# Kernel optimization log

Measured on AMD Instinct MI355X. Metric: run time of the kernel, lower is better.

The kernel has to match this reference:

```python
import jax, jax.numpy as jnp
import numpy as np
import math

B, S, D, H, FF, L, V = 4, 2048, 512, 8, 2048, 4, 256
WINDOW, STRIDE, NGLOBAL = 256, 128, 16  # sparse pattern: causal & (local | strided | global)


def setup_inputs() -> dict:
    key = jax.random.key(0)
    ks = jax.random.split(key, 12)
    g = lambda k, shp: jax.random.normal(k, shp, dtype=jnp.float32) * 0.02
    return {
        "src_tokens": jax.random.randint(ks[0], (B, S), 0, V, dtype=jnp.int32),
        "emb": g(ks[1], (V, D)),
        "b_out": jnp.zeros((V,), jnp.float32),
        "Wq": g(ks[2], (L, D, D)), "bq": jnp.zeros((L, D), jnp.float32),
        "Wk": g(ks[3], (L, D, D)), "bk": jnp.zeros((L, D), jnp.float32),
        "Wv": g(ks[4], (L, D, D)), "bv": jnp.zeros((L, D), jnp.float32),
        "Wo": g(ks[5], (L, D, D)), "bo": jnp.zeros((L, D), jnp.float32),
        "ln1_g": jnp.ones((L, D), jnp.float32), "ln1_b": jnp.zeros((L, D), jnp.float32),
        "W1": g(ks[6], (L, D, FF)), "b1": jnp.zeros((L, FF), jnp.float32),
        "W2": g(ks[7], (L, FF, D)), "b2": jnp.zeros((L, D), jnp.float32),
        "ln2_g": jnp.ones((L, D), jnp.float32), "ln2_b": jnp.zeros((L, D), jnp.float32),
    }


def _pos_enc(seq_len, d_model):
    pos = jnp.arange(seq_len, dtype=jnp.float32)[:, None]
    div = jnp.exp(jnp.arange(0, d_model, 2, dtype=jnp.float32) * (-math.log(10000.0) / d_model))
    pe = jnp.zeros((seq_len, d_model), jnp.float32)
    pe = pe.at[:, 0::2].set(jnp.sin(pos * div)).at[:, 1::2].set(jnp.cos(pos * div))
    return pe


def _ln(x, g, b):
    m = x.mean(-1, keepdims=True)
    v = ((x - m) ** 2).mean(-1, keepdims=True)
    return (x - m) * jax.lax.rsqrt(v + 1e-5) * g + b


def _sparse_mask(seq_len):
    i = jnp.arange(seq_len)[:, None]
    j = jnp.arange(seq_len)[None, :]
    causal = j <= i
    local = (i - j) < WINDOW
    strided = ((i - j) % STRIDE) == 0
    glob = j < NGLOBAL
    return causal & (local | strided | glob)  # [S, S] bool


def reference(src_tokens, emb, b_out, Wq, bq, Wk, bk, Wv, bv, Wo, bo,
              ln1_g, ln1_b, W1, b1, W2, b2, ln2_g, ln2_b):
    dh = D // H
    x = emb[src_tokens] * math.sqrt(D) + _pos_enc(S, D)  # [B,S,D] (dropout inactive at eval)
    mask = _sparse_mask(S)
    for l in range(L):
        q = (x @ Wq[l] + bq[l]).reshape(B, S, H, dh)
        k = (x @ Wk[l] + bk[l]).reshape(B, S, H, dh)
        v = (x @ Wv[l] + bv[l]).reshape(B, S, H, dh)
        scores = jnp.einsum('bihd,bjhd->bhij', q, k) / math.sqrt(dh)
        scores = jnp.where(mask, scores, jnp.float32(-1e9))
        attn = jax.nn.softmax(scores, axis=-1)
        o = jnp.einsum('bhij,bjhd->bihd', attn, v).reshape(B, S, D)
        x = _ln(x + o @ Wo[l] + bo[l], ln1_g[l], ln1_b[l])      # post-LN residual
        h = jax.nn.relu(x @ W1[l] + b1[l])
        x = _ln(x + h @ W2[l] + b2[l], ln2_g[l], ln2_b[l])
    return x @ emb.T + b_out  # tied output projection -> [B,S,V]
```

## Files before the change

kernel.cpp:

```cpp
#include <hip/hip_runtime.h>
#include <hip/hip_bf16.h>
#include <math.h>

#define B_  4
#define S_  2048
#define D_  512
#define H_  8
#define DH_ 64
#define FF_ 2048
#define L_  4
#define V_  256
#define NTOK (B_ * S_)
#define XN  ((size_t)NTOK * D_)

typedef __attribute__((ext_vector_type(8))) short bf16x8;
typedef __attribute__((ext_vector_type(4))) float f32x4;
typedef __attribute__((ext_vector_type(8))) unsigned short u16x8;
typedef __attribute__((ext_vector_type(4))) unsigned short u16x4;

typedef const __attribute__((address_space(1))) unsigned int* gptr_u32;
typedef __attribute__((address_space(3))) unsigned int* lptr_u32;

__device__ __forceinline__ float bf2f(unsigned short u) {
    return __uint_as_float((unsigned)u << 16);
}
__device__ __forceinline__ unsigned short f2bf_bits(float f) {
    __hip_bfloat16 t = __float2bfloat16(f);
    return *(unsigned short*)&t;
}

__global__ void pe_table_kernel(float* __restrict__ PE) {
    int s = blockIdx.x;
    int d = threadIdx.x * 2;
    float ang = (float)s * expf((float)d * (-logf(10000.0f) / (float)D_));
    PE[(size_t)s * D_ + d]     = sinf(ang);
    PE[(size_t)s * D_ + d + 1] = cosf(ang);
}

__global__ void embed_kernel(const int* __restrict__ tok,
                             const float* __restrict__ emb,
                             const float* __restrict__ PE,
                             float* __restrict__ X,
                             __hip_bfloat16* __restrict__ Xb) {
    int bs = blockIdx.x;
    int s = bs % S_;
    int t = tok[bs];
    const float scale = 22.62741699796952f;
    int d = threadIdx.x * 4;
    float4 e = *(const float4*)(emb + (size_t)t * D_ + d);
    float4 p = *(const float4*)(PE + (size_t)s * D_ + d);
    float4 v = make_float4(e.x * scale + p.x, e.y * scale + p.y,
                           e.z * scale + p.z, e.w * scale + p.w);
    *(float4*)(X + (size_t)bs * D_ + d) = v;
    u16x4 pk = { f2bf_bits(v.x), f2bf_bits(v.y), f2bf_bits(v.z), f2bf_bits(v.w) };
    *(u16x4*)((unsigned short*)Xb + (size_t)bs * D_ + d) = pk;
}

__global__ void transpose_conv_kernel(const float* __restrict__ W,
                                      __hip_bfloat16* __restrict__ Wt,
                                      int K, int N) {
    const float* Wl = W + (size_t)blockIdx.z * K * N;
    __hip_bfloat16* Wtl = Wt + (size_t)blockIdx.z * K * N;
    __shared__ float t[32][33];
    int k0 = blockIdx.y * 32, n0 = blockIdx.x * 32;
    int tx = threadIdx.x & 31, ty = threadIdx.x >> 5;
    #pragma unroll
    for (int q = 0; q < 4; ++q)
        t[ty + q * 8][tx] = Wl[(size_t)(k0 + ty + q * 8) * N + n0 + tx];
    __syncthreads();
    #pragma unroll
    for (int q = 0; q < 4; ++q)
        Wtl[(size_t)(n0 + ty + q * 8) * K + k0 + tx] =
            __float2bfloat16(t[tx][ty + q * 8]);
}

__global__ void transpose_qkv_kernel(const float* __restrict__ Wq,
                                     const float* __restrict__ Wk,
                                     const float* __restrict__ Wv,
                                     __hip_bfloat16* __restrict__ dst) {
    int z = blockIdx.z, l = z / 3, which = z % 3;
    const float* src = (which == 0 ? Wq : which == 1 ? Wk : Wv) + (size_t)l * D_ * D_;
    __hip_bfloat16* d = dst + (size_t)l * 1536 * D_ + (size_t)which * D_ * D_;
    __shared__ float t[32][33];
    int k0 = blockIdx.y * 32, n0 = blockIdx.x * 32;
    int tx = threadIdx.x & 31, ty = threadIdx.x >> 5;
    #pragma unroll
    for (int q = 0; q < 4; ++q)
        t[ty + q * 8][tx] = src[(size_t)(k0 + ty + q * 8) * D_ + n0 + tx];
    __syncthreads();
    #pragma unroll
    for (int q = 0; q < 4; ++q)
        d[(size_t)(n0 + ty + q * 8) * D_ + k0 + tx] =
            __float2bfloat16(t[tx][ty + q * 8]);
}

__global__ void conv_bf16_kernel(const float* __restrict__ in,
                                 __hip_bfloat16* __restrict__ out, int n) {
    int i = blockIdx.x * 256 + threadIdx.x;
    if (i < n) out[i] = __float2bfloat16(in[i]);
}

template <int BM, int RELU, int OUT_MODE>
__global__ __launch_bounds__(256)
void gemm_bf16_kernel(const __hip_bfloat16* __restrict__ A,
                      const __hip_bfloat16* __restrict__ Bt,
                      const float* __restrict__ bias0,
                      const float* __restrict__ bias1,
                      const float* __restrict__ bias2,
                      float* __restrict__ Cf,
                      __hip_bfloat16* __restrict__ Cb0,
                      __hip_bfloat16* __restrict__ Cb1,
                      __hip_bfloat16* __restrict__ Cb2,
                      __hip_bfloat16* __restrict__ CbT,
                      int M, int N, int K) {
    constexpr int MI = BM / 32;
    __shared__ unsigned short As[2][BM * 32];
    __shared__ unsigned short Bs[2][128 * 32];
    int tid = threadIdx.x;
    int lane = tid & 63, wid = tid >> 6;
    int wm = (wid >> 1) * (BM / 2), wn = (wid & 1) * 64;
    int g = lane >> 4, il = lane & 15;

    int gx = gridDim.x;
    int fid = blockIdx.x + gx * blockIdx.y;
    int cpx = (gx * gridDim.y) >> 3;
    int swz = (fid & 7) * cpx + (fid >> 3);
    int m0 = (swz / gx) * BM, n0 = (swz % gx) * 128;

    auto stage = [&](int buf, int k0) {
        #pragma unroll
        for (int q = 0; q < BM / 64; ++q) {
            int idx = q * 256 + tid;
            int r = idx >> 2, c = idx & 3;
            int csw = (c ^ r) & 3;
            const __hip_bfloat16* sa = A + (size_t)(m0 + r) * K + k0 + csw * 8;
            __builtin_amdgcn_global_load_lds((gptr_u32)(const void*)sa,
                                             (lptr_u32)(void*)&As[buf][idx * 8], 16, 0, 0);
        }
        #pragma unroll
        for (int q = 0; q < 2; ++q) {
            int idx = q * 256 + tid;
            int r = idx >> 2, c = idx & 3;
            int csw = (c ^ r) & 3;
            const __hip_bfloat16* sb = Bt + (size_t)(n0 + r) * K + k0 + csw * 8;
            __builtin_amdgcn_global_load_lds((gptr_u32)(const void*)sb,
                                             (lptr_u32)(void*)&Bs[buf][idx * 8], 16, 0, 0);
        }
    };

    f32x4 acc[MI][4] = {};
    int NT = K >> 5;
    stage(0, 0);

    for (int t = 0; t < NT; ++t) {
        int cur = t & 1;
        if (t + 1 < NT) {
            stage(cur ^ 1, (t + 1) << 5);
            if constexpr (BM == 128)
                asm volatile("s_waitcnt vmcnt(4)" ::: "memory");
            else
                asm volatile("s_waitcnt vmcnt(3)" ::: "memory");
        } else {
            asm volatile("s_waitcnt vmcnt(0)" ::: "memory");
        }
        __builtin_amdgcn_s_barrier();

        bf16x8 af[MI], bf[4];
        #pragma unroll
        for (int i = 0; i < MI; ++i) {
            int m = wm + i * 16 + il;
            af[i] = *(const bf16x8*)&As[cur][m * 32 + ((g ^ m) & 3) * 8];
        }
        #pragma unroll
        for (int j = 0; j < 4; ++j) {
            int n = wn + j * 16 + il;
            bf[j] = *(const bf16x8*)&Bs[cur][n * 32 + ((g ^ n) & 3) * 8];
        }
        #pragma unroll
        for (int i = 0; i < MI; ++i)
            #pragma unroll
            for (int j = 0; j < 4; ++j)
                acc[i][j] = __builtin_amdgcn_mfma_f32_16x16x32_bf16(
                    af[i], bf[j], acc[i][j], 0, 0, 0);

        __builtin_amdgcn_s_barrier();
    }

    if constexpr (OUT_MODE == 4) {
        int seg = n0 >> 9;
        const float* bias = seg == 0 ? bias0 : seg == 1 ? bias1 : bias2;
        __hip_bfloat16* Crow = seg == 0 ? Cb0 : seg == 1 ? Cb1 : Cb2;
        int nseg = n0 & 511;
        #pragma unroll
        for (int j = 0; j < 4; ++j) {
            int coll = nseg + wn + j * 16 + il;
            float bv = bias[coll];
            #pragma unroll
            for (int i = 0; i < MI; ++i) {
                int row0 = m0 + wm + i * 16 + g * 4;
                if (seg < 2) {
                    #pragma unroll
                    for (int r = 0; r < 4; ++r)
                        Crow[(size_t)(row0 + r) * 512 + coll] =
                            __float2bfloat16(acc[i][j][r] + bv);
                } else {
                    u16x4 pk;
                    #pragma unroll
                    for (int r = 0; r < 4; ++r) {
                        float v = acc[i][j][r] + bv;
                        Crow[(size_t)(row0 + r) * 512 + coll] = __float2bfloat16(v);
                        pk[r] = f2bf_bits(v);
                    }
                    int hh = coll >> 6, dh = coll & 63;
                    int bb = row0 >> 11, s0 = row0 & 2047;
                    *(u16x4*)(CbT + ((size_t)((bb * 8 + hh) * 64 + dh) * 2048 + s0)) = pk;
                }
            }
        }
    } else {
        #pragma unroll
        for (int j = 0; j < 4; ++j) {
            int col = n0 + wn + j * 16 + il;
            float bv = bias0[col];
            #pragma unroll
            for (int i = 0; i < MI; ++i) {
                #pragma unroll
                for (int r = 0; r < 4; ++r) {
                    int row = m0 + wm + i * 16 + g * 4 + r;
                    float v = acc[i][j][r] + bv;
                    if (RELU) v = fmaxf(v, 0.0f);
                    if (OUT_MODE == 1) Cb0[(size_t)row * N + col] = __float2bfloat16(v);
                    else               Cf[(size_t)row * N + col] = v;
                }
            }
        }
    }
}

__device__ __forceinline__ bf16x8 lds_frag(const unsigned short* base, int row, int chunk) {
    int byte = (row << 7) + (((chunk ^ (row & 7)) & 7) << 4);
    return *(const bf16x8*)((const char*)base + byte);
}

__global__ __launch_bounds__(256)
void attn_mfma_kernel(const __hip_bfloat16* __restrict__ Q,
                      const __hip_bfloat16* __restrict__ K,
                      const __hip_bfloat16* __restrict__ V,
                      const __hip_bfloat16* __restrict__ VT,
                      __hip_bfloat16* __restrict__ O) {
    __shared__ unsigned short SM[4096 + 4096 + 4096];
    unsigned short* Ks = SM;
    unsigned short* Vs = SM + 4096;

    int d = blockIdx.x + 32 * (blockIdx.y + 8 * blockIdx.z);
    int xcd = d & 7;
    int rest = d >> 3;
    int gsub = rest & 3;
    int qt = rest >> 2;
    int grp = xcd * 4 + gsub;
    int h = grp & 7, b = grp >> 3;
    int i0 = qt * 64;

    int tid = threadIdx.x, lane = tid & 63, wv = tid >> 6;
    int g = lane >> 4, il = lane & 15, g4 = g * 4;

    int nloc = min(i0 >> 6, 4) + 1;
    int add0 = (i0 > 256);
    int nt = nloc + add0;

    const size_t vt_off = (size_t)((b * 8 + h) * 64) * 2048;
    auto j0_of = [&](int t) { return (t < nloc) ? (i0 - 64 * t) : 0; };

    auto stage = [&](int j0) {
        #pragma unroll
        for (int q = 0; q < 2; ++q) {
            int idx = q * 256 + tid;
            int row = idx >> 3, c = idx & 7;
            int csw = c ^ (row & 7);
            const __hip_bfloat16* sk = K + (size_t)(b * 2048 + j0 + row) * 512 + h * 64 + csw * 8;
            __builtin_amdgcn_global_load_lds((gptr_u32)(const void*)sk,
                                             (lptr_u32)(void*)&Ks[idx * 8], 16, 0, 0);
            const __hip_bfloat16* sv = VT + vt_off + (size_t)row * 2048 + j0 + csw * 8;
            __builtin_amdgcn_global_load_lds((gptr_u32)(const void*)sv,
                                             (lptr_u32)(void*)&Vs[idx * 8], 16, 0, 0);
        }
    };

    int iq = i0 + wv * 16 + il;
    bf16x8 qf[2];
    #pragma unroll
    for (int kh = 0; kh < 2; ++kh)
        qf[kh] = *(const bf16x8*)(Q + (size_t)(b * 2048 + iq) * 512 + h * 64 + kh * 32 + g * 8);

    stage(j0_of(0));

    float qfl[16];
    #pragma unroll
    for (int kh = 0; kh < 2; ++kh)
        #pragma unroll
        for (int e = 0; e < 8; ++e)
            qfl[kh * 8 + e] = bf2f(((u16x8)qf[kh])[e]);

    unsigned short* myP = SM + 8192 + wv * 1024;
    f32x4 o[4] = {};
    float os[16] = {};
    float m = -1e30f, l = 0.0f;
    const float CSC = 0.18033688011112042f;

    const unsigned short* Kbase = (const unsigned short*)(K + (size_t)b * 2048 * 512 + h * 64);
    const unsigned short* Vbase = (const unsigned short*)(V + (size_t)b * 2048 * 512 + h * 64);
    for (int j = iq - 384; j >= 16; j -= 128) {
        const unsigned short* kr = Kbase + (size_t)j * 512;
        u16x8 k0 = *(const u16x8*)(kr + g * 8);
        u16x8 k1 = *(const u16x8*)(kr + 32 + g * 8);
        float dot = 0.0f;
        #pragma unroll
        for (int e = 0; e < 8; ++e)
            dot += qfl[e] * bf2f(k0[e]) + qfl[8 + e] * bf2f(k1[e]);
        dot += __shfl_xor(dot, 16);
        dot += __shfl_xor(dot, 32);
        float s2 = dot * CSC;
        float mn = fmaxf(m, s2);
        float al = exp2f(m - mn);
        float p = exp2f(s2 - mn);
        l = l * al + p;
        m = mn;
        const unsigned short* vr = Vbase + (size_t)j * 512;
        u16x8 v0 = *(const u16x8*)(vr + g * 8);
        u16x8 v1 = *(const u16x8*)(vr + 32 + g * 8);
        #pragma unroll
        for (int e = 0; e < 8; ++e) {
            os[e]     = os[e]     * al + p * bf2f(v0[e]);
            os[8 + e] = os[8 + e] * al + p * bf2f(v1[e]);
        }
    }

    for (int t = 0; t < nt; ++t) {
        asm volatile("s_waitcnt vmcnt(0)" ::: "memory");
        __builtin_amdgcn_s_barrier();
        int j0 = j0_of(t);
        bool gtile = (t >= nloc);
        bool dtile = (t == 0);

        f32x4 s[4] = {};
        __builtin_amdgcn_s_setprio(1);
        if (gtile) {
            #pragma unroll
            for (int kh = 0; kh < 2; ++kh) {
                bf16x8 a = lds_frag(Ks, il, kh * 4 + g);
                s[0] = __builtin_amdgcn_mfma_f32_16x16x32_bf16(a, qf[kh], s[0], 0, 0, 0);
            }
        } else if (dtile) {
            #pragma unroll
            for (int kh = 0; kh < 2; ++kh)
                #pragma unroll
                for (int jn = 0; jn < 4; ++jn)
                    if (jn <= wv) {
                        bf16x8 a = lds_frag(Ks, jn * 16 + il, kh * 4 + g);
                        s[jn] = __builtin_amdgcn_mfma_f32_16x16x32_bf16(a, qf[kh], s[jn], 0, 0, 0);
                    }
        } else {
            #pragma unroll
            for (int kh = 0; kh < 2; ++kh)
                #pragma unroll
                for (int jn = 0; jn < 4; ++jn) {
                    bf16x8 a = lds_frag(Ks, jn * 16 + il, kh * 4 + g);
                    s[jn] = __builtin_amdgcn_mfma_f32_16x16x32_bf16(a, qf[kh], s[jn], 0, 0, 0);
                }
        }
        __builtin_amdgcn_s_setprio(0);

        float mloc = -1e30f;
        if (gtile) {
            #pragma unroll
            for (int r = 0; r < 4; ++r) {
                float sv = s[0][r] * CSC;
                s[0][r] = sv;
                mloc = fmaxf(mloc, sv);
            }
        } else if (dtile) {
            #pragma unroll
            for (int jn = 0; jn < 4; ++jn) {
                if (jn < wv) {
                    #pragma unroll
                    for (int r = 0; r < 4; ++r) {
                        float sv = s[jn][r] * CSC;
                        s[jn][r] = sv;
                        mloc = fmaxf(mloc, sv);
                    }
                } else if (jn == wv) {
                    #pragma unroll
                    for (int r = 0; r < 4; ++r) {
                        float sv = (g4 + r <= il) ? s[jn][r] * CSC : -1e30f;
                        s[jn][r] = sv;
                        mloc = fmaxf(mloc, sv);
                    }
                }
            }
        } else if (t == 4) {
            #pragma unroll
            for (int jn = 0; jn < 4; ++jn)
                #pragma unroll
                for (int r = 0; r < 4; ++r) {
                    int jg = j0 + jn * 16 + g4 + r;
                    int dij = iq - jg;
                    bool ok = (dij < 256) || ((dij & 127) == 0) || (jg < 16);
                    float sv = ok ? s[jn][r] * CSC : -1e30f;
                    s[jn][r] = sv;
                    mloc = fmaxf(mloc, sv);
                }
        } else {
            #pragma unroll
            for (int jn = 0; jn < 4; ++jn)
                #pragma unroll
                for (int r = 0; r < 4; ++r) {
                    float sv = s[jn][r] * CSC;
                    s[jn][r] = sv;
                    mloc = fmaxf(mloc, sv);
                }
        }
        mloc = fmaxf(mloc, __shfl_xor(mloc, 16));
        mloc = fmaxf(mloc, __shfl_xor(mloc, 32));
        float mn = fmaxf(m, mloc);
        float al = exp2f(m - mn);

        float lloc = 0.0f;
        if (gtile) {
            #pragma unroll
            for (int r = 0; r < 4; ++r) {
                float p = exp2f(s[0][r] - mn);
                s[0][r] = p;
                lloc += p;
            }
        } else {
            #pragma unroll
            for (int jn = 0; jn < 4; ++jn) {
                if (dtile && jn > wv) continue;
                #pragma unroll
                for (int r = 0; r < 4; ++r) {
                    float p = exp2f(s[jn][r] - mn);
                    s[jn][r] = p;
                    lloc += p;
                }
            }
        }
        lloc += __shfl_xor(lloc, 16);
        lloc += __shfl_xor(lloc, 32);
        l = l * al + lloc;
        m = mn;

        if (!__all(al == 1.0f)) {
            float ar[4];
            #pragma unroll
            for (int r = 0; r < 4; ++r) ar[r] = __shfl(al, g4 + r);
            #pragma unroll
            for (int dn = 0; dn < 4; ++dn)
                #pragma unroll
                for (int r = 0; r < 4; ++r) o[dn][r] *= ar[r];
            #pragma unroll
            for (int e = 0; e < 16; ++e) os[e] *= al;
        }

        #pragma unroll
        for (int jn = 0; jn < 4; ++jn) {
            if (gtile && jn >= 2) continue;
            u16x4 pk = { 0, 0, 0, 0 };
            bool live = gtile ? (jn == 0) : (!dtile || jn <= wv);
            if (live) {
                #pragma unroll
                for (int r = 0; r < 4; ++r) pk[r] = f2bf_bits(s[jn][r]);
            }
            int byte = ((il << 7) + (jn << 5) + (g << 3)) ^ ((il & 7) << 4);
            *(u16x4*)((char*)myP + byte) = pk;
        }
        int khmax = (gtile || (dtile && wv < 2)) ? 1 : 2;
        __builtin_amdgcn_s_setprio(1);
        #pragma unroll
        for (int kh = 0; kh < 2; ++kh) {
            if (kh < khmax) {
                bf16x8 pa = lds_frag(myP, il, kh * 4 + g);
                #pragma unroll
                for (int dn = 0; dn < 4; ++dn) {
                    bf16x8 bv = lds_frag(Vs, dn * 16 + il, kh * 4 + g);
                    o[dn] = __builtin_amdgcn_mfma_f32_16x16x32_bf16(pa, bv, o[dn], 0, 0, 0);
                }
            }
        }
        __builtin_amdgcn_s_setprio(0);

        __builtin_amdgcn_s_barrier();
        if (t + 1 < nt) stage(j0_of(t + 1));
    }

    float* osl = (float*)SM + wv * 1024;
    #pragma unroll
    for (int kh = 0; kh < 2; ++kh)
        #pragma unroll
        for (int e = 0; e < 8; ++e)
            osl[il * 64 + kh * 32 + g * 8 + e] = os[kh * 8 + e];
    __syncthreads();

    float li[4];
    #pragma unroll
    for (int r = 0; r < 4; ++r) li[r] = 1.0f / __shfl(l, g4 + r);
    #pragma unroll
    for (int dn = 0; dn < 4; ++dn)
        #pragma unroll
        for (int r = 0; r < 4; ++r) {
            int row = i0 + wv * 16 + g4 + r;
            float add = osl[(g4 + r) * 64 + dn * 16 + il];
            O[(size_t)(b * 2048 + row) * 512 + h * 64 + dn * 16 + il] =
                __float2bfloat16((o[dn][r] + add) * li[r]);
        }
}

__global__ __launch_bounds__(256)
void add_ln_kernel(float* __restrict__ X,
                   const __hip_bfloat16* __restrict__ T,
                   const float* __restrict__ g,
                   const float* __restrict__ bb,
                   __hip_bfloat16* __restrict__ Xb) {
    size_t row = blockIdx.x * 4 + (threadIdx.x >> 6);
    int lane = threadIdx.x & 63;
    int d0 = lane * 8;
    float4 x0 = *(const float4*)(X + row * D_ + d0);
    float4 x1 = *(const float4*)(X + row * D_ + d0 + 4);
    u16x8 tv = *(const u16x8*)((const unsigned short*)T + row * D_ + d0);
    float v[8] = { x0.x + bf2f(tv[0]), x0.y + bf2f(tv[1]),
                   x0.z + bf2f(tv[2]), x0.w + bf2f(tv[3]),
                   x1.x + bf2f(tv[4]), x1.y + bf2f(tv[5]),
                   x1.z + bf2f(tv[6]), x1.w + bf2f(tv[7]) };
    float sum = 0.0f;
    #pragma unroll
    for (int q = 0; q < 8; ++q) sum += v[q];
    #pragma unroll
    for (int o = 32; o; o >>= 1) sum += __shfl_xor(sum, o);
    float mean = sum * (1.0f / D_);
    float var = 0.0f;
    #pragma unroll
    for (int q = 0; q < 8; ++q) { float dd = v[q] - mean; var += dd * dd; }
    #pragma unroll
    for (int o = 32; o; o >>= 1) var += __shfl_xor(var, o);
    var *= (1.0f / D_);
    float r = rsqrtf(var + 1e-5f);
    float4 g0 = *(const float4*)(g + d0),  g1 = *(const float4*)(g + d0 + 4);
    float4 b0 = *(const float4*)(bb + d0), b1 = *(const float4*)(bb + d0 + 4);
    float y[8];
    y[0] = (v[0]-mean)*r*g0.x+b0.x; y[1] = (v[1]-mean)*r*g0.y+b0.y;
    y[2] = (v[2]-mean)*r*g0.z+b0.z; y[3] = (v[3]-mean)*r*g0.w+b0.w;
    y[4] = (v[4]-mean)*r*g1.x+b1.x; y[5] = (v[5]-mean)*r*g1.y+b1.y;
    y[6] = (v[6]-mean)*r*g1.z+b1.z; y[7] = (v[7]-mean)*r*g1.w+b1.w;
    *(float4*)(X + row * D_ + d0)     = make_float4(y[0], y[1], y[2], y[3]);
    *(float4*)(X + row * D_ + d0 + 4) = make_float4(y[4], y[5], y[6], y[7]);
    u16x8 pk;
    #pragma unroll
    for (int q = 0; q < 8; ++q) pk[q] = f2bf_bits(y[q]);
    *(u16x8*)((unsigned short*)Xb + row * D_ + d0) = pk;
}

extern "C" void kernel_launch(void* const* d_in, const int* in_sizes, int n_in,
                              void* d_out, int out_size, void* d_ws, size_t ws_size,
                              hipStream_t stream) {
    const int*   tok   = (const int*)  d_in[0];
    const float* emb   = (const float*)d_in[1];
    const float* b_out = (const float*)d_in[2];
    const float* Wq    = (const float*)d_in[3];
    const float* bq    = (const float*)d_in[4];
    const float* Wk    = (const float*)d_in[5];
    const float* bk    = (const float*)d_in[6];
    const float* Wv    = (const float*)d_in[7];
    const float* bv    = (const float*)d_in[8];
    const float* Wo    = (const float*)d_in[9];
    const float* bo    = (const float*)d_in[10];
    const float* ln1g  = (const float*)d_in[11];
    const float* ln1b  = (const float*)d_in[12];
    const float* W1    = (const float*)d_in[13];
    const float* b1    = (const float*)d_in[14];
    const float* W2    = (const float*)d_in[15];
    const float* b2    = (const float*)d_in[16];
    const float* ln2g  = (const float*)d_in[17];
    const float* ln2b  = (const float*)d_in[18];
    float* out = (float*)d_out;

    char* w = (char*)d_ws;
    auto alloc = [&](size_t bytes) {
        char* p = w;
        w += (bytes + 255) & ~(size_t)255;
        return p;
    };
    float*          X   = (float*)         alloc(XN * 4);
    __hip_bfloat16* Xb  = (__hip_bfloat16*)alloc(XN * 2);
    __hip_bfloat16* Tb  = (__hip_bfloat16*)alloc(XN * 2);
    char* uni = alloc(XN * 2 * 5);
    __hip_bfloat16* Qb  = (__hip_bfloat16*)uni;
    __hip_bfloat16* Kb  = Qb + XN;
    __hip_bfloat16* Vb  = Kb + XN;
    __hip_bfloat16* VTb = Vb + XN;
    __hip_bfloat16* Ob  = VTb + XN;
    __hip_bfloat16* Hb  = (__hip_bfloat16*)uni;
    __hip_bfloat16* Wqkvt = (__hip_bfloat16*)alloc((size_t)L_ * 1536 * D_ * 2);
    __hip_bfloat16* Wot  = (__hip_bfloat16*)alloc((size_t)L_ * D_ * D_ * 2);
    __hip_bfloat16* W1t  = (__hip_bfloat16*)alloc((size_t)L_ * D_ * FF_ * 2);
    __hip_bfloat16* W2t  = (__hip_bfloat16*)alloc((size_t)L_ * FF_ * D_ * 2);
    __hip_bfloat16* embb = (__hip_bfloat16*)alloc((size_t)V_ * D_ * 2);
    float*          PE   = (float*)alloc((size_t)S_ * D_ * 4);

    {
        pe_table_kernel<<<S_, 256, 0, stream>>>(PE);
        dim3 gqkv(D_ / 32, D_ / 32, L_ * 3);
        transpose_qkv_kernel<<<gqkv, 256, 0, stream>>>(Wq, Wk, Wv, Wqkvt);
        dim3 gdd(D_ / 32, D_ / 32, L_);
        transpose_conv_kernel<<<gdd, 256, 0, stream>>>(Wo, Wot, D_, D_);
        dim3 g1(FF_ / 32, D_ / 32, L_);
        transpose_conv_kernel<<<g1, 256, 0, stream>>>(W1, W1t, D_, FF_);
        dim3 g2(D_ / 32, FF_ / 32, L_);
        transpose_conv_kernel<<<g2, 256, 0, stream>>>(W2, W2t, FF_, D_);
        conv_bf16_kernel<<<(V_ * D_ + 255) / 256, 256, 0, stream>>>(emb, embb, V_ * D_);
    }

    embed_kernel<<<NTOK, 128, 0, stream>>>(tok, emb, PE, X, Xb);

    dim3 blk(256);
    dim3 gqkv(1536 / 128, NTOK / 128);
    dim3 g512n(D_ / 128, NTOK / 64);
    dim3 gff (FF_ / 128, NTOK / 128);
    dim3 gout(V_ / 128, NTOK / 64);
    dim3 gattn(S_ / 64, H_, B_);
    dim3 gln(NTOK / 4);

    for (int l = 0; l < L_; ++l) {
        const __hip_bfloat16* wqkv = Wqkvt + (size_t)l * 1536 * D_;
        const __hip_bfloat16* wot = Wot + (size_t)l * D_ * D_;
        const __hip_bfloat16* w1t = W1t + (size_t)l * D_ * FF_;
        const __hip_bfloat16* w2t = W2t + (size_t)l * FF_ * D_;

        gemm_bf16_kernel<128, 0, 4><<<gqkv, blk, 0, stream>>>(
            Xb, wqkv, bq + l * D_, bk + l * D_, bv + l * D_,
            nullptr, Qb, Kb, Vb, VTb, NTOK, 1536, D_);

        attn_mfma_kernel<<<gattn, blk, 0, stream>>>(Qb, Kb, Vb, VTb, Ob);

        gemm_bf16_kernel<64, 0, 1><<<g512n, blk, 0, stream>>>(
            Ob, wot, bo + l * D_, nullptr, nullptr,
            nullptr, Tb, nullptr, nullptr, nullptr, NTOK, D_, D_);
        add_ln_kernel<<<gln, blk, 0, stream>>>(X, Tb, ln1g + l * D_, ln1b + l * D_, Xb);

        gemm_bf16_kernel<128, 1, 1><<<gff, blk, 0, stream>>>(
            Xb, w1t, b1 + l * FF_, nullptr, nullptr,
            nullptr, Hb, nullptr, nullptr, nullptr, NTOK, FF_, D_);
        gemm_bf16_kernel<64, 0, 1><<<g512n, blk, 0, stream>>>(
            Hb, w2t, b2 + l * D_, nullptr, nullptr,
            nullptr, Tb, nullptr, nullptr, nullptr, NTOK, D_, FF_);
        add_ln_kernel<<<gln, blk, 0, stream>>>(X, Tb, ln2g + l * D_, ln2b + l * D_, Xb);
    }

    gemm_bf16_kernel<64, 0, 0><<<gout, blk, 0, stream>>>(
        Xb, embb, b_out, nullptr, nullptr,
        out, nullptr, nullptr, nullptr, nullptr, NTOK, V_, D_);
}
```

Before: 655.1 us.

## Split-K the Wo and W2 GEMMs into two halves summed in add_ln

The output-projection and FFN-down GEMMs now run with a third grid dimension of 2. Each z-slice computes half of the K reduction and writes its own bf16 partial result into free scratch buffers (the Q and O slots). The add_ln kernel reads both partials and sums them with the residual. This doubles the block count and halves per-block K-loop length for these narrow-N GEMMs, to fill more CUs. The cost is an extra partial write and read, plus a second bf16 rounding of each partial.

```diff
diff --git a/kernel.cpp b/kernel.cpp
--- a/kernel.cpp
+++ b/kernel.cpp
@@ -112,7 +112,7 @@
                       __hip_bfloat16* __restrict__ Cb1,
                       __hip_bfloat16* __restrict__ Cb2,
                       __hip_bfloat16* __restrict__ CbT,
-                      int M, int N, int K) {
+                      int M, int N, int K, int lda) {
     constexpr int MI = BM / 32;
     __shared__ unsigned short As[2][BM * 32];
     __shared__ unsigned short Bs[2][128 * 32];
@@ -127,13 +127,16 @@
     int swz = (fid & 7) * cpx + (fid >> 3);
     int m0 = (swz / gx) * BM, n0 = (swz % gx) * 128;
 
+    size_t koff = 0;
+    if constexpr (OUT_MODE == 5) koff = (size_t)blockIdx.z * K;
+
     auto stage = [&](int buf, int k0) {
         #pragma unroll
         for (int q = 0; q < BM / 64; ++q) {
             int idx = q * 256 + tid;
             int r = idx >> 2, c = idx & 3;
             int csw = (c ^ r) & 3;
-            const __hip_bfloat16* sa = A + (size_t)(m0 + r) * K + k0 + csw * 8;
+            const __hip_bfloat16* sa = A + (size_t)(m0 + r) * lda + koff + k0 + csw * 8;
             __builtin_amdgcn_global_load_lds((gptr_u32)(const void*)sa,
                                              (lptr_u32)(void*)&As[buf][idx * 8], 16, 0, 0);
         }
@@ -142,7 +145,7 @@
             int idx = q * 256 + tid;
             int r = idx >> 2, c = idx & 3;
             int csw = (c ^ r) & 3;
-            const __hip_bfloat16* sb = Bt + (size_t)(n0 + r) * K + k0 + csw * 8;
+            const __hip_bfloat16* sb = Bt + (size_t)(n0 + r) * lda + koff + k0 + csw * 8;
             __builtin_amdgcn_global_load_lds((gptr_u32)(const void*)sb,
                                              (lptr_u32)(void*)&Bs[buf][idx * 8], 16, 0, 0);
         }
@@ -217,6 +220,21 @@
                 }
             }
         }
+    } else if constexpr (OUT_MODE == 5) {
+        __hip_bfloat16* Cd = blockIdx.z ? Cb1 : Cb0;
+        #pragma unroll
+        for (int j = 0; j < 4; ++j) {
+            int col = n0 + wn + j * 16 + il;
+            float bv = blockIdx.z ? 0.0f : bias0[col];
+            #pragma unroll
+            for (int i = 0; i < MI; ++i) {
+                #pragma unroll
+                for (int r = 0; r < 4; ++r) {
+                    int row = m0 + wm + i * 16 + g * 4 + r;
+                    Cd[(size_t)row * N + col] = __float2bfloat16(acc[i][j][r] + bv);
+                }
+            }
+        }
     } else {
         #pragma unroll
         for (int j = 0; j < 4; ++j) {
@@ -516,7 +534,8 @@
 
 __global__ __launch_bounds__(256)
 void add_ln_kernel(float* __restrict__ X,
-                   const __hip_bfloat16* __restrict__ T,
+                   const __hip_bfloat16* __restrict__ T1,
+                   const __hip_bfloat16* __restrict__ T2,
                    const float* __restrict__ g,
                    const float* __restrict__ bb,
                    __hip_bfloat16* __restrict__ Xb) {
@@ -525,11 +544,12 @@
     int d0 = lane * 8;
     float4 x0 = *(const float4*)(X + row * D_ + d0);
     float4 x1 = *(const float4*)(X + row * D_ + d0 + 4);
-    u16x8 tv = *(const u16x8*)((const unsigned short*)T + row * D_ + d0);
-    float v[8] = { x0.x + bf2f(tv[0]), x0.y + bf2f(tv[1]),
-                   x0.z + bf2f(tv[2]), x0.w + bf2f(tv[3]),
-                   x1.x + bf2f(tv[4]), x1.y + bf2f(tv[5]),
-                   x1.z + bf2f(tv[6]), x1.w + bf2f(tv[7]) };
+    u16x8 t1 = *(const u16x8*)((const unsigned short*)T1 + row * D_ + d0);
+    u16x8 t2 = *(const u16x8*)((const unsigned short*)T2 + row * D_ + d0);
+    float v[8] = { x0.x + bf2f(t1[0]) + bf2f(t2[0]), x0.y + bf2f(t1[1]) + bf2f(t2[1]),
+                   x0.z + bf2f(t1[2]) + bf2f(t2[2]), x0.w + bf2f(t1[3]) + bf2f(t2[3]),
+                   x1.x + bf2f(t1[4]) + bf2f(t2[4]), x1.y + bf2f(t1[5]) + bf2f(t2[5]),
+                   x1.z + bf2f(t1[6]) + bf2f(t2[6]), x1.w + bf2f(t1[7]) + bf2f(t2[7]) };
     float sum = 0.0f;
     #pragma unroll
     for (int q = 0; q < 8; ++q) sum += v[q];
@@ -598,6 +618,8 @@
     __hip_bfloat16* VTb = Vb + XN;
     __hip_bfloat16* Ob  = VTb + XN;
     __hip_bfloat16* Hb  = (__hip_bfloat16*)uni;
+    __hip_bfloat16* T2wo = Qb;
+    __hip_bfloat16* T2w2 = Ob;
     __hip_bfloat16* Wqkvt = (__hip_bfloat16*)alloc((size_t)L_ * 1536 * D_ * 2);
     __hip_bfloat16* Wot  = (__hip_bfloat16*)alloc((size_t)L_ * D_ * D_ * 2);
     __hip_bfloat16* W1t  = (__hip_bfloat16*)alloc((size_t)L_ * D_ * FF_ * 2);
@@ -622,7 +644,7 @@
 
     dim3 blk(256);
     dim3 gqkv(1536 / 128, NTOK / 128);
-    dim3 g512n(D_ / 128, NTOK / 64);
+    dim3 gsplit(D_ / 128, NTOK / 64, 2);
     dim3 gff (FF_ / 128, NTOK / 128);
     dim3 gout(V_ / 128, NTOK / 64);
     dim3 gattn(S_ / 64, H_, B_);
@@ -636,25 +658,26 @@
 
         gemm_bf16_kernel<128, 0, 4><<<gqkv, blk, 0, stream>>>(
             Xb, wqkv, bq + l * D_, bk + l * D_, bv + l * D_,
-            nullptr, Qb, Kb, Vb, VTb, NTOK, 1536, D_);
+            nullptr, Qb, Kb, Vb, VTb, NTOK, 1536, D_, D_);
 
         attn_mfma_kernel<<<gattn, blk, 0, stream>>>(Qb, Kb, Vb, VTb, Ob);
 
-        gemm_bf16_kernel<64, 0, 1><<<g512n, blk, 0, stream>>>(
+        gemm_bf16_kernel<64, 0, 5><<<gsplit, blk, 0, stream>>>(
             Ob, wot, bo + l * D_, nullptr, nullptr,
-            nullptr, Tb, nullptr, nullptr, nullptr, NTOK, D_, D_);
-        add_ln_kernel<<<gln, blk, 0, stream>>>(X, Tb, ln1g + l * D_, ln1b + l * D_, Xb);
+            nullptr, Tb, T2wo, nullptr, nullptr, NTOK, D_, 256, D_);
+        add_ln_kernel<<<gln, blk, 0, stream>>>(X, Tb, T2wo, ln1g + l * D_, ln1b + l * D_, Xb);
 
         gemm_bf16_kernel<128, 1, 1><<<gff, blk, 0, stream>>>(
             Xb, w1t, b1 + l * FF_, nullptr, nullptr,
-            nullptr, Hb, nullptr, nullptr, nullptr, NTOK, FF_, D_);
-        gemm_bf16_kernel<64, 0, 1><<<g512n, blk, 0, stream>>>(
+            nullptr, Hb, nullptr, nullptr, nullptr, NTOK, FF_, D_, D_);
+
+        gemm_bf16_kernel<64, 0, 5><<<gsplit, blk, 0, stream>>>(
             Hb, w2t, b2 + l * D_, nullptr, nullptr,
-            nullptr, Tb, nullptr, nullptr, nullptr, NTOK, D_, FF_);
-        add_ln_kernel<<<gln, blk, 0, stream>>>(X, Tb, ln2g + l * D_, ln2b + l * D_, Xb);
+            nullptr, Tb, T2w2, nullptr, nullptr, NTOK, D_, 1024, FF_);
+        add_ln_kernel<<<gln, blk, 0, stream>>>(X, Tb, T2w2, ln2g + l * D_, ln2b + l * D_, Xb);
     }
 
     gemm_bf16_kernel<64, 0, 0><<<gout, blk, 0, stream>>>(
         Xb, embb, b_out, nullptr, nullptr,
-        out, nullptr, nullptr, nullptr, nullptr, NTOK, V_, D_);
-}
+        out, nullptr, nullptr, nullptr, nullptr, NTOK, V_, D_, D_);
+}
```

After: 656.4 us. About the same (+0.2%).
